# Performance work log

Measured on AMD Instinct MI355X. Metric: run time of the kernel, lower is better.

## Reference

```python
import jax, jax.numpy as jnp
import numpy as np

B, NV, CIN, C = 1, 40000, 128, 64
D, H, W = 19, 200, 176  # sparse_shape = output_shape[1:4] + [1,0,0]
EPS = 1e-3
DN = ('NCDHW', 'OIDHW', 'NCDHW')


def setup_inputs():
    key = jax.random.key(0)
    ks = jax.random.split(key, 12)
    vf = jax.random.normal(ks[0], (NV, CIN), jnp.float32)
    bi = jnp.zeros((NV, 1), jnp.int32)
    zi = jax.random.randint(ks[1], (NV, 1), 0, D, jnp.int32)
    yi = jax.random.randint(ks[2], (NV, 1), 0, H, jnp.int32)
    xi = jax.random.randint(ks[3], (NV, 1), 0, W, jnp.int32)
    coors = jnp.concatenate([bi, zi, yi, xi], axis=1)  # [batch, z, y, x]
    s = 0.05
    w_sub1 = jax.random.normal(ks[4], (C, CIN, 3, 3, 3), jnp.float32) * s
    w_down1 = jax.random.normal(ks[5], (C, C, 3, 1, 1), jnp.float32) * s
    w_sub2 = jax.random.normal(ks[6], (C, C, 3, 3, 3), jnp.float32) * s
    w_sub3 = jax.random.normal(ks[7], (C, C, 3, 3, 3), jnp.float32) * s
    w_down2 = jax.random.normal(ks[8], (C, C, 3, 1, 1), jnp.float32) * s
    bn_gamma = 1.0 + 0.1 * jax.random.normal(ks[9], (5, C), jnp.float32)
    bn_beta = 0.1 * jax.random.normal(ks[10], (5, C), jnp.float32)
    bn_mean = 0.1 * jax.random.normal(ks[11], (5, C), jnp.float32)
    bn_var = jnp.ones((5, C), jnp.float32)
    return dict(voxel_features=vf, coors=coors, batch_size=1,
                w_sub1=w_sub1, w_down1=w_down1, w_sub2=w_sub2, w_sub3=w_sub3,
                w_down2=w_down2, bn_gamma=bn_gamma, bn_beta=bn_beta,
                bn_mean=bn_mean, bn_var=bn_var)


def _conv(x, w, stride, pad):
    return jax.lax.conv_general_dilated(x, w, stride, pad, dimension_numbers=DN)


def _bnrelu(x, i, mask, g, b, m, v):
    # eval-mode BN on active sites only (inactive sites stay exactly zero -> mask)
    inv = jax.lax.rsqrt(v[i] + EPS)
    y = (x - m[i][None, :, None, None, None]) * (g[i] * inv)[None, :, None, None, None] \
        + b[i][None, :, None, None, None]
    return jnp.maximum(y, 0.0) * mask


def _forward(voxel_features, coors, batch_size, w_sub1, w_down1, w_sub2, w_sub3,
             w_down2, bn_gamma, bn_beta, bn_mean, bn_var):
    bi, zi, yi, xi = coors[:, 0], coors[:, 1], coors[:, 2], coors[:, 3]
    # scn.InputLayer: scatter (sum duplicates) active voxel features into dense grid
    dense = jnp.zeros((batch_size, D, H, W, CIN), voxel_features.dtype)
    dense = dense.at[bi, zi, yi, xi].add(voxel_features)
    x = jnp.transpose(dense, (0, 4, 1, 2, 3))  # NCDHW
    mask = jnp.zeros((batch_size, D, H, W), voxel_features.dtype)
    mask = mask.at[bi, zi, yi, xi].set(1.0)[:, None]  # [B,1,D,H,W] active sites
    ones_k = jnp.ones((1, 1, 3, 1, 1), x.dtype)
    pad1 = ((1, 1), (1, 1), (1, 1))
    bn = (bn_gamma, bn_beta, bn_mean, bn_var)
    # SubmanifoldConvolution(128->64, k3) + BNReLU : output only at active sites
    x = _bnrelu(_conv(x, w_sub1, (1, 1, 1), pad1) * mask, 0, mask, *bn)
    # Convolution 64->64 kernel (3,1,1) stride (2,1,1): new active set = any input in window
    x = _conv(x, w_down1, (2, 1, 1), 'VALID')
    mask = (_conv(mask, ones_k, (2, 1, 1), 'VALID') > 0).astype(x.dtype)
    x = _bnrelu(x, 1, mask, *bn)
    # two more submanifold convs
    x = _bnrelu(_conv(x, w_sub2, (1, 1, 1), pad1) * mask, 2, mask, *bn)
    x = _bnrelu(_conv(x, w_sub3, (1, 1, 1), pad1) * mask, 3, mask, *bn)
    # second strided conv
    x = _conv(x, w_down2, (2, 1, 1), 'VALID')
    mask = (_conv(mask, ones_k, (2, 1, 1), 'VALID') > 0).astype(x.dtype)
    x = _bnrelu(x, 4, mask, *bn)
    # SparseToDense then view(N, C*D, H, W)
    Nb, Cc, Dd, Hh, Ww = x.shape
    return x.reshape(Nb, Cc * Dd, Hh, Ww)


def reference(voxel_features, coors, batch_size, w_sub1, w_down1, w_sub2, w_sub3,
              w_down2, bn_gamma, bn_beta, bn_mean, bn_var):
    return _forward(voxel_features, coors, batch_size, w_sub1, w_down1, w_sub2,
                    w_sub3, w_down2, bn_gamma, bn_beta, bn_mean, bn_var)
```

## Files before the change

kernel.cpp:

```cpp
#include <hip/hip_runtime.h>

typedef float floatx4 __attribute__((ext_vector_type(4)));
typedef _Float16 f16x8 __attribute__((ext_vector_type(8)));

#define D0_ 19
#define H0_ 200
#define W0_ 176
#define HW_ (H0_*W0_)
#define NCELL0 (D0_*HW_)
#define D1_ 9
#define NCELL1 (D1_*HW_)
#define D2_ 4
#define NCELL2 (D2_*HW_)
#define NV_ 40000
#define CAP0 40000
#define CAP1 80000
#define CAP2 140800
#define EPS_ 1e-3f

typedef __attribute__((address_space(1))) const unsigned int* gas_t;
typedef __attribute__((address_space(3))) unsigned int* las_t;

__device__ __forceinline__ short f2h(float f){
    _Float16 h = (_Float16)f;
    short s; __builtin_memcpy(&s, &h, 2); return s;
}

__device__ __forceinline__ void repack_one(const float* w, short* Bout, int i,
                                           int KCsrc, int kshift, int NSP){
    int k = i >> 6, n = i & 63;
    int j = k >> kshift;
    int ci = k & (KCsrc - 1);
    short val = f2h(w[(n * KCsrc + ci) * NSP + j]);
    int chunk = k >> 5, lanehi = (k >> 3) & 3, jj = k & 7;
    int nt = n >> 4, lane = lanehi * 16 + (n & 15);
    Bout[((chunk * 4 + nt) * 64 + lane) * 8 + jj] = val;
}

#define RP1 (3456*64)
#define RP2 (1728*64)
#define RPD (192*64)

__global__ void k_prep(const float* w1, const float* w2, const float* w3,
                       const float* wd1, const float* wd2,
                       short* B1, short* B2, short* B3, short* Bd1, short* Bd2,
                       const float* g, const float* b, const float* m, const float* v,
                       float* scale, float* shift){
    int i = blockIdx.x * 256 + threadIdx.x;
    if (i < RP1){ repack_one(w1, B1, i, 128, 7, 27); return; }
    i -= RP1;
    if (i < RP2){ repack_one(w2, B2, i, 64, 6, 27); return; }
    i -= RP2;
    if (i < RP2){ repack_one(w3, B3, i, 64, 6, 27); return; }
    i -= RP2;
    if (i < RPD){ repack_one(wd1, Bd1, i, 64, 6, 3); return; }
    i -= RPD;
    if (i < RPD){ repack_one(wd2, Bd2, i, 64, 6, 3); return; }
    i -= RPD;
    if (i < 5*64){
        float s = g[i] / sqrtf(v[i] + EPS_);
        scale[i] = s;
        shift[i] = b[i] - m[i] * s;
    }
}
#define PREP_TOT (RP1 + 2*RP2 + 2*RPD + 5*64)

__global__ void k_count(const int* coors, int* cntg){
    int v = blockIdx.x * 256 + threadIdx.x;
    if (v >= NV_) return;
    int z = coors[v*4+1], y = coors[v*4+2], x = coors[v*4+3];
    atomicAdd(&cntg[(z*H0_ + y)*W0_ + x], 1);
}

__device__ __forceinline__ int blk_rank(bool act, int* cnt, int& r_out){
    unsigned long long mask = __ballot(act);
    int lane = threadIdx.x & 63, wid = threadIdx.x >> 6;
    int wrank = __popcll(mask & ((1ull << lane) - 1));
    __shared__ int ws[4];
    __shared__ int blkbase;
    if (lane == 0) ws[wid] = __popcll(mask);
    __syncthreads();
    if (threadIdx.x == 0){
        int t0 = ws[0], t1 = ws[1], t2 = ws[2], t3 = ws[3];
        int tot = t0 + t1 + t2 + t3;
        blkbase = tot ? atomicAdd(cnt, tot) : 0;
        ws[0] = 0; ws[1] = t0; ws[2] = t0 + t1; ws[3] = t0 + t1 + t2;
    }
    __syncthreads();
    r_out = blkbase + ws[wid] + wrank;
    return 0;
}

__global__ void k_compact0(const int* cntg, int* idx0, int* list0, int* cnt0){
    int c = blockIdx.x * 256 + threadIdx.x;
    bool act = (c < NCELL0) && (cntg[c] > 0);
    int r; blk_rank(act, cnt0, r);
    if (c >= NCELL0) return;
    if (act){
        idx0[c] = r;
        int z = c / HW_; int rem = c - z * HW_;
        int y = rem / W0_; int x = rem - y * W0_;
        list0[r] = (z << 16) | (y << 8) | x;
    } else idx0[c] = -1;
}

__global__ void k_compact_dn(const int* idxsrc, int* idxdst, int* listdst, int* cnt,
                             int ncell){
    int c = blockIdx.x * 256 + threadIdx.x;
    bool act = false;
    int d = 0, y = 0, x = 0;
    if (c < ncell){
        d = c / HW_; int rem = c - d * HW_;
        y = rem / W0_; x = rem - y * W0_;
        #pragma unroll
        for (int j = 0; j < 3; ++j)
            act = act || (idxsrc[((2*d + j)*H0_ + y)*W0_ + x] >= 0);
    }
    int r; blk_rank(act, cnt, r);
    if (c >= ncell) return;
    if (act){
        idxdst[c] = r;
        listdst[r] = (d << 16) | (y << 8) | x;
    } else idxdst[c] = -1;
}

__global__ void k_scatter(const float* vf, const int* coors, const int* cntg,
                          const int* idx0, float* feat0f){
    int u = blockIdx.x * 256 + threadIdx.x;
    if (u >= NV_ * 32) return;
    int v = u >> 5, c4 = u & 31;
    int z = coors[v*4+1], y = coors[v*4+2], x = coors[v*4+3];
    int cell = (z*H0_ + y)*W0_ + x;
    int row = idx0[cell];
    float4 s = ((const float4*)(vf + (long)v * 128))[c4];
    float* dst = feat0f + (long)row * 128 + c4 * 4;
    if (cntg[cell] == 1){
        *(float4*)dst = s;
    } else {
        atomicAdd(dst+0, s.x); atomicAdd(dst+1, s.y);
        atomicAdd(dst+2, s.z); atomicAdd(dst+3, s.w);
    }
}

__global__ void k_convert(const float* f, short* b, const int* cntp){
    int n8 = cntp[0] * 16;
    int i = blockIdx.x * 256 + threadIdx.x;
    if (i >= n8) return;
    float4 a = ((const float4*)f)[i*2], c = ((const float4*)f)[i*2+1];
    short o[8] = { f2h(a.x), f2h(a.y), f2h(a.z), f2h(a.w),
                   f2h(c.x), f2h(c.y), f2h(c.z), f2h(c.w) };
    ((int4*)b)[i] = *(int4*)o;
}

__global__ void k_nbrs(const int* list0, const int* list1, const int* list2,
                       const int* idx0, const int* idx1,
                       int* nbr0T, int* nbr1T, int* dnb1T, int* dnb2T,
                       const int* counters){
    int job = blockIdx.z;
    int j = blockIdx.y;
    int site = blockIdx.x * 256 + threadIdx.x;
    if (job < 2){
        int M = counters[job];
        if (site >= M) return;
        const int* list = job ? list1 : list0;
        const int* idxg = job ? idx1 : idx0;
        int Dd = job ? D1_ : D0_;
        int cap = job ? CAP1 : CAP0;
        int cell = list[site];
        int z = cell >> 16, y = (cell >> 8) & 255, x = cell & 255;
        int nz = z + j/9 - 1, ny = y + (j/3)%3 - 1, nx = x + j%3 - 1;
        int r = -1;
        if ((unsigned)nz < (unsigned)Dd && (unsigned)ny < H0_ && (unsigned)nx < W0_)
            r = idxg[(nz*H0_ + ny)*W0_ + nx];
        (job ? nbr1T : nbr0T)[j * cap + site] = r;
    } else {
        if (j >= 3) return;
        int lvl = job - 2;
        int M = counters[lvl + 1];
        if (site >= M) return;
        const int* list = lvl ? list2 : list1;
        const int* idxg = lvl ? idx1 : idx0;
        int cap = lvl ? CAP2 : CAP1;
        int cell = list[site];
        int d = cell >> 16, y = (cell >> 8) & 255, x = cell & 255;
        (lvl ? dnb2T : dnb1T)[j * cap + site] = idxg[((2*d + j)*H0_ + y)*W0_ + x];
    }
}

template<int NNBR, int NCH, bool FINAL>
__global__ __launch_bounds__(256) void k_gemm(
    const short* __restrict__ featA, const int* __restrict__ nbrT, int nstride,
    const short* __restrict__ Bs, short* __restrict__ out,
    const int* __restrict__ cntp,
    const float* __restrict__ scale, const float* __restrict__ shift,
    const int* __restrict__ list, float* __restrict__ dout)
{
    __shared__ short Blds[2][NCH*4*512];
    int M = *cntp;
    int m0 = blockIdx.x * 64;
    if (m0 >= M) return;
    int tid = threadIdx.x;
    int wave = tid >> 6, lane = tid & 63;
    int m16 = lane & 15;
    int koff = (lane >> 4) * 8;
    const int ROWS = NCH * 32;
    const int FPW = NCH;

    int row = m0 + wave * 16 + m16;
    bool ok = row < M;

    floatx4 acc[4] = {};
    f16x8 A[2][NCH];
    const f16x8 z8 = {0,0,0,0,0,0,0,0};

    auto stageB = [&](int j, int b){
        #pragma unroll
        for (int f = 0; f < FPW; ++f){
            int frag = wave * FPW + f;
            const short* g = Bs + (((long)j * NCH * 4 + frag) * 64 + lane) * 8;
            __builtin_amdgcn_global_load_lds((gas_t)g, (las_t)&Blds[b][frag * 512],
                                             16, 0, 0);
        }
    };
    auto loadA1 = [&](f16x8* dst, int r, int kc){
        dst[kc] = (r >= 0) ? *(const f16x8*)(featA + (long)r*ROWS + koff + kc*32) : z8;
    };

    int rc = ok ? nbrT[row] : -1;
    stageB(0, 0);
    #pragma unroll
    for (int kc = 0; kc < NCH; ++kc) loadA1(A[0], rc, kc);
    int rb = (NNBR > 1 && ok) ? nbrT[nstride + row] : -1;
    int ra = -1;
    __syncthreads();

    #pragma unroll
    for (int t = 0; t < NNBR; ++t){
        if (t + 1 < NNBR){
            stageB(t + 1, (t + 1) & 1);
            #pragma unroll
            for (int kc = 0; kc < NCH; ++kc) loadA1(A[(t+1)&1], rb, kc);
        }
        if (t + 2 < NNBR)
            ra = ok ? nbrT[(t+2)*nstride + row] : -1;
        if (__ballot(rc >= 0) != 0){
            const short* Bb = Blds[t & 1];
            #pragma unroll
            for (int kc = 0; kc < NCH; ++kc){
                f16x8 b[4];
                #pragma unroll
                for (int nt = 0; nt < 4; ++nt)
                    b[nt] = *(const f16x8*)&Bb[((kc*4 + nt) * 64 + lane) * 8];
                f16x8 a = A[t&1][kc];
                #pragma unroll
                for (int nt = 0; nt < 4; ++nt)
                    acc[nt] = __builtin_amdgcn_mfma_f32_16x16x32_f16(a, b[nt], acc[nt], 0, 0, 0);
            }
        }
        rc = rb; rb = ra;
        __syncthreads();
    }

    int n16 = lane & 15;
    int mb = m0 + wave * 16 + (lane >> 4) * 4;
    #pragma unroll
    for (int nt = 0; nt < 4; ++nt){
        int n = nt * 16 + n16;
        float sc = scale[n], sh = shift[n];
        #pragma unroll
        for (int r = 0; r < 4; ++r){
            int site = mb + r;
            if (site < M){
                float y = fmaxf(acc[nt][r] * sc + sh, 0.f);
                if (FINAL){
                    int cell = list[site];
                    int d = cell >> 16, yy = (cell >> 8) & 255, xx = cell & 255;
                    dout[((n*4 + d)*H0_ + yy)*W0_ + xx] = y;
                } else {
                    out[(long)site*64 + n] = f2h(y);
                }
            }
        }
    }
}

extern "C" void kernel_launch(void* const* d_in, const int* in_sizes, int n_in,
                              void* d_out, int out_size, void* d_ws, size_t ws_size,
                              hipStream_t stream){
    const float* vf   = (const float*)d_in[0];
    const int*   coors= (const int*)  d_in[1];
    const float* w1   = (const float*)d_in[3];
    const float* wd1  = (const float*)d_in[4];
    const float* w2   = (const float*)d_in[5];
    const float* w3   = (const float*)d_in[6];
    const float* wd2  = (const float*)d_in[7];
    const float* bng  = (const float*)d_in[8];
    const float* bnb  = (const float*)d_in[9];
    const float* bnm  = (const float*)d_in[10];
    const float* bnv  = (const float*)d_in[11];
    float* dout = (float*)d_out;

    char* ws = (char*)d_ws;
    size_t off = 0;
    auto alloc = [&](size_t bytes)->char* {
        char* p = ws + off;
        off += (bytes + 255) & ~(size_t)255;
        return p;
    };

    int*   counters = (int*)  alloc(256);
    int*   cntg     = (int*)  alloc((size_t)NCELL0 * 4);
    int*   idx0     = (int*)  alloc((size_t)NCELL0 * 4);
    int*   idx1     = (int*)  alloc((size_t)NCELL1 * 4);
    int*   idx2     = (int*)  alloc((size_t)NCELL2 * 4);
    int*   list0    = (int*)  alloc((size_t)CAP0 * 4);
    int*   list1    = (int*)  alloc((size_t)CAP1 * 4);
    int*   list2    = (int*)  alloc((size_t)CAP2 * 4);
    float* feat0f   = (float*)alloc((size_t)CAP0 * 128 * 4);
    short* feat0h   = (short*)alloc((size_t)CAP0 * 128 * 2);
    short* feat1    = (short*)alloc((size_t)CAP0 * 64 * 2);
    short* featd1   = (short*)alloc((size_t)CAP1 * 64 * 2);
    short* feat2    = (short*)alloc((size_t)CAP1 * 64 * 2);
    short* feat3    = (short*)alloc((size_t)CAP1 * 64 * 2);
    int*   nbr0T    = (int*)  alloc((size_t)CAP0 * 27 * 4);
    int*   nbr1T    = (int*)  alloc((size_t)CAP1 * 27 * 4);
    int*   dnb1T    = (int*)  alloc((size_t)CAP1 * 3 * 4);
    int*   dnb2T    = (int*)  alloc((size_t)CAP2 * 3 * 4);
    short* B1  = (short*)alloc((size_t)3456 * 64 * 2);
    short* B2  = (short*)alloc((size_t)1728 * 64 * 2);
    short* B3  = (short*)alloc((size_t)1728 * 64 * 2);
    short* Bd1 = (short*)alloc((size_t)192 * 64 * 2);
    short* Bd2 = (short*)alloc((size_t)192 * 64 * 2);
    float* bnscale = (float*)alloc(5 * 64 * 4);
    float* bnshift = (float*)alloc(5 * 64 * 4);

    hipMemsetAsync(counters, 0, 256 + (size_t)NCELL0 * 4, stream);
    hipMemsetAsync(feat0f, 0, (size_t)CAP0 * 128 * 4, stream);
    hipMemsetAsync(dout, 0, (size_t)out_size * 4, stream);

    k_prep<<<(PREP_TOT + 255)/256, 256, 0, stream>>>(w1, w2, w3, wd1, wd2,
        B1, B2, B3, Bd1, Bd2, bng, bnb, bnm, bnv, bnscale, bnshift);

    k_count<<<(NV_ + 255)/256, 256, 0, stream>>>(coors, cntg);
    k_compact0<<<(NCELL0 + 255)/256, 256, 0, stream>>>(cntg, idx0, list0, counters + 0);
    k_scatter<<<(NV_*32 + 255)/256, 256, 0, stream>>>(vf, coors, cntg, idx0, feat0f);
    k_convert<<<(CAP0*16 + 255)/256, 256, 0, stream>>>(feat0f, feat0h, counters + 0);
    k_compact_dn<<<(NCELL1 + 255)/256, 256, 0, stream>>>(idx0, idx1, list1, counters + 1, NCELL1);
    k_compact_dn<<<(NCELL2 + 255)/256, 256, 0, stream>>>(idx1, idx2, list2, counters + 2, NCELL2);

    dim3 gn((CAP2 + 255)/256, 27, 4);
    k_nbrs<<<gn, 256, 0, stream>>>(list0, list1, list2, idx0, idx1,
                                   nbr0T, nbr1T, dnb1T, dnb2T, counters);

    k_gemm<27,4,false><<<(CAP0+63)/64, 256, 0, stream>>>(feat0h, nbr0T, CAP0, B1, feat1,
        counters + 0, bnscale + 0,   bnshift + 0,   nullptr, nullptr);
    k_gemm<3,2,false><<<(CAP1+63)/64, 256, 0, stream>>>(feat1, dnb1T, CAP1, Bd1, featd1,
        counters + 1, bnscale + 64,  bnshift + 64,  nullptr, nullptr);
    k_gemm<27,2,false><<<(CAP1+63)/64, 256, 0, stream>>>(featd1, nbr1T, CAP1, B2, feat2,
        counters + 1, bnscale + 128, bnshift + 128, nullptr, nullptr);
    k_gemm<27,2,false><<<(CAP1+63)/64, 256, 0, stream>>>(feat2, nbr1T, CAP1, B3, feat3,
        counters + 1, bnscale + 192, bnshift + 192, nullptr, nullptr);
    k_gemm<3,2,true><<<(CAP2+63)/64, 256, 0, stream>>>(feat3, dnb2T, CAP2, Bd2, nullptr,
        counters + 2, bnscale + 256, bnshift + 256, list2, dout);
}
```

Measured before the change: 318.0 us.

## Compute neighbor indices inline in GEMM kernels and fold voxel counting into prep

Removes the separate neighbor-table kernel and its index tables. Each GEMM now computes neighbor indices on the fly from the site's coordinates and the dense index grid, using a 3-deep A-register pipeline so the index lookup runs ahead of the feature load. The voxel-count atomics are merged into the weight-repack prep kernel, saving one launch. In exchange, the 27-tap index lookups are recomputed in each of the three submanifold GEMMs (the two level-1 convs share the same neighbors), and the lookup latency now sits inside the GEMM loop. More A registers are also live per thread.

```diff
diff --git a/kernel.cpp b/kernel.cpp
--- a/kernel.cpp
+++ b/kernel.cpp
@@ -45,7 +45,8 @@
                        const float* wd1, const float* wd2,
                        short* B1, short* B2, short* B3, short* Bd1, short* Bd2,
                        const float* g, const float* b, const float* m, const float* v,
-                       float* scale, float* shift){
+                       float* scale, float* shift,
+                       const int* coors, int* cntg){
     int i = blockIdx.x * 256 + threadIdx.x;
     if (i < RP1){ repack_one(w1, B1, i, 128, 7, 27); return; }
     i -= RP1;
@@ -61,16 +62,15 @@
         float s = g[i] / sqrtf(v[i] + EPS_);
         scale[i] = s;
         shift[i] = b[i] - m[i] * s;
-    }
-}
-#define PREP_TOT (RP1 + 2*RP2 + 2*RPD + 5*64)
-
-__global__ void k_count(const int* coors, int* cntg){
-    int v = blockIdx.x * 256 + threadIdx.x;
-    if (v >= NV_) return;
-    int z = coors[v*4+1], y = coors[v*4+2], x = coors[v*4+3];
-    atomicAdd(&cntg[(z*H0_ + y)*W0_ + x], 1);
-}
+        return;
+    }
+    i -= 5*64;
+    if (i < NV_){
+        int z = coors[i*4+1], y = coors[i*4+2], x = coors[i*4+3];
+        atomicAdd(&cntg[(z*H0_ + y)*W0_ + x], 1);
+    }
+}
+#define PREP_TOT (RP1 + 2*RP2 + 2*RPD + 5*64 + NV_)
 
 __device__ __forceinline__ int blk_rank(bool act, int* cnt, int& r_out){
     unsigned long long mask = __ballot(act);
@@ -152,50 +152,17 @@
     ((int4*)b)[i] = *(int4*)o;
 }
 
-__global__ void k_nbrs(const int* list0, const int* list1, const int* list2,
-                       const int* idx0, const int* idx1,
-                       int* nbr0T, int* nbr1T, int* dnb1T, int* dnb2T,
-                       const int* counters){
-    int job = blockIdx.z;
-    int j = blockIdx.y;
-    int site = blockIdx.x * 256 + threadIdx.x;
-    if (job < 2){
-        int M = counters[job];
-        if (site >= M) return;
-        const int* list = job ? list1 : list0;
-        const int* idxg = job ? idx1 : idx0;
-        int Dd = job ? D1_ : D0_;
-        int cap = job ? CAP1 : CAP0;
-        int cell = list[site];
-        int z = cell >> 16, y = (cell >> 8) & 255, x = cell & 255;
-        int nz = z + j/9 - 1, ny = y + (j/3)%3 - 1, nx = x + j%3 - 1;
-        int r = -1;
-        if ((unsigned)nz < (unsigned)Dd && (unsigned)ny < H0_ && (unsigned)nx < W0_)
-            r = idxg[(nz*H0_ + ny)*W0_ + nx];
-        (job ? nbr1T : nbr0T)[j * cap + site] = r;
-    } else {
-        if (j >= 3) return;
-        int lvl = job - 2;
-        int M = counters[lvl + 1];
-        if (site >= M) return;
-        const int* list = lvl ? list2 : list1;
-        const int* idxg = lvl ? idx1 : idx0;
-        int cap = lvl ? CAP2 : CAP1;
-        int cell = list[site];
-        int d = cell >> 16, y = (cell >> 8) & 255, x = cell & 255;
-        (lvl ? dnb2T : dnb1T)[j * cap + site] = idxg[((2*d + j)*H0_ + y)*W0_ + x];
-    }
-}
-
-template<int NNBR, int NCH, bool FINAL>
-__global__ __launch_bounds__(256) void k_gemm(
-    const short* __restrict__ featA, const int* __restrict__ nbrT, int nstride,
+template<int NCH>
+__global__ __launch_bounds__(256) void k_gemm27(
+    const short* __restrict__ featA, const int* __restrict__ list,
+    const int* __restrict__ idxg, int Dd,
     const short* __restrict__ Bs, short* __restrict__ out,
     const int* __restrict__ cntp,
-    const float* __restrict__ scale, const float* __restrict__ shift,
-    const int* __restrict__ list, float* __restrict__ dout)
+    const float* __restrict__ scale, const float* __restrict__ shift)
 {
     __shared__ short Blds[2][NCH*4*512];
+    constexpr int NT = 27;
+    const int ROWS = NCH * 32;
     int M = *cntp;
     int m0 = blockIdx.x * 64;
     if (m0 >= M) return;
@@ -203,47 +170,50 @@
     int wave = tid >> 6, lane = tid & 63;
     int m16 = lane & 15;
     int koff = (lane >> 4) * 8;
-    const int ROWS = NCH * 32;
-    const int FPW = NCH;
 
     int row = m0 + wave * 16 + m16;
     bool ok = row < M;
+    int cell = ok ? list[row] : 0xFF0000;
+    int z = cell >> 16, y = (cell >> 8) & 255, x = cell & 255;
 
     floatx4 acc[4] = {};
-    f16x8 A[2][NCH];
+    f16x8 A[3][NCH];
     const f16x8 z8 = {0,0,0,0,0,0,0,0};
 
     auto stageB = [&](int j, int b){
         #pragma unroll
-        for (int f = 0; f < FPW; ++f){
-            int frag = wave * FPW + f;
+        for (int f = 0; f < NCH; ++f){
+            int frag = wave * NCH + f;
             const short* g = Bs + (((long)j * NCH * 4 + frag) * 64 + lane) * 8;
             __builtin_amdgcn_global_load_lds((gas_t)g, (las_t)&Blds[b][frag * 512],
                                              16, 0, 0);
         }
     };
-    auto loadA1 = [&](f16x8* dst, int r, int kc){
-        dst[kc] = (r >= 0) ? *(const f16x8*)(featA + (long)r*ROWS + koff + kc*32) : z8;
-    };
-
-    int rc = ok ? nbrT[row] : -1;
+    auto getR = [&](int t)->int{
+        int nz = z + t/9 - 1, ny = y + (t/3)%3 - 1, nx = x + t%3 - 1;
+        int r = -1;
+        if ((unsigned)nz < (unsigned)Dd && (unsigned)ny < H0_ && (unsigned)nx < W0_)
+            r = idxg[(nz*H0_ + ny)*W0_ + nx];
+        return r;
+    };
+    auto loadA = [&](f16x8* dst, int r){
+        #pragma unroll
+        for (int kc = 0; kc < NCH; ++kc)
+            dst[kc] = (r >= 0) ? *(const f16x8*)(featA + (long)r*ROWS + koff + kc*32) : z8;
+    };
+
+    int r0 = getR(0), r1 = getR(1), r2 = getR(2);
     stageB(0, 0);
+    loadA(A[0], r0);
+    loadA(A[1], r1);
+    __syncthreads();
+
     #pragma unroll
-    for (int kc = 0; kc < NCH; ++kc) loadA1(A[0], rc, kc);
-    int rb = (NNBR > 1 && ok) ? nbrT[nstride + row] : -1;
-    int ra = -1;
-    __syncthreads();
-
-    #pragma unroll
-    for (int t = 0; t < NNBR; ++t){
-        if (t + 1 < NNBR){
-            stageB(t + 1, (t + 1) & 1);
-            #pragma unroll
-            for (int kc = 0; kc < NCH; ++kc) loadA1(A[(t+1)&1], rb, kc);
-        }
-        if (t + 2 < NNBR)
-            ra = ok ? nbrT[(t+2)*nstride + row] : -1;
-        if (__ballot(rc >= 0) != 0){
+    for (int t = 0; t < NT; ++t){
+        if (t + 1 < NT) stageB(t + 1, (t + 1) & 1);
+        if (t + 2 < NT) loadA(A[(t + 2) % 3], r2);
+        int rn = (t + 3 < NT) ? getR(t + 3) : -1;
+        if (__ballot(r0 >= 0) != 0){
             const short* Bb = Blds[t & 1];
             #pragma unroll
             for (int kc = 0; kc < NCH; ++kc){
@@ -251,13 +221,13 @@
                 #pragma unroll
                 for (int nt = 0; nt < 4; ++nt)
                     b[nt] = *(const f16x8*)&Bb[((kc*4 + nt) * 64 + lane) * 8];
-                f16x8 a = A[t&1][kc];
+                f16x8 a = A[t % 3][kc];
                 #pragma unroll
                 for (int nt = 0; nt < 4; ++nt)
                     acc[nt] = __builtin_amdgcn_mfma_f32_16x16x32_f16(a, b[nt], acc[nt], 0, 0, 0);
             }
         }
-        rc = rb; rb = ra;
+        r0 = r1; r1 = r2; r2 = rn;
         __syncthreads();
     }
 
@@ -270,14 +240,109 @@
         #pragma unroll
         for (int r = 0; r < 4; ++r){
             int site = mb + r;
+            if (site < M)
+                out[(long)site*64 + n] = f2h(fmaxf(acc[nt][r] * sc + sh, 0.f));
+        }
+    }
+}
+
+template<bool FINAL>
+__global__ __launch_bounds__(256) void k_gemmdn(
+    const short* __restrict__ featA, const int* __restrict__ list,
+    const int* __restrict__ idxg, int parentD,
+    const short* __restrict__ Bs, short* __restrict__ out,
+    const int* __restrict__ cntp,
+    const float* __restrict__ scale, const float* __restrict__ shift,
+    float* __restrict__ dout)
+{
+    __shared__ short Blds[2][2*4*512];
+    constexpr int NT = 3;
+    const int ROWS = 64;
+    int M = *cntp;
+    int m0 = blockIdx.x * 64;
+    if (m0 >= M) return;
+    int tid = threadIdx.x;
+    int wave = tid >> 6, lane = tid & 63;
+    int m16 = lane & 15;
+    int koff = (lane >> 4) * 8;
+
+    int row = m0 + wave * 16 + m16;
+    bool ok = row < M;
+    int cell = ok ? list[row] : 0;
+    int d = ok ? (cell >> 16) : 300;
+    int y = (cell >> 8) & 255, x = cell & 255;
+
+    floatx4 acc[4] = {};
+    f16x8 A[3][2];
+    const f16x8 z8 = {0,0,0,0,0,0,0,0};
+
+    auto stageB = [&](int j, int b){
+        #pragma unroll
+        for (int f = 0; f < 2; ++f){
+            int frag = wave * 2 + f;
+            const short* g = Bs + (((long)j * 8 + frag) * 64 + lane) * 8;
+            __builtin_amdgcn_global_load_lds((gas_t)g, (las_t)&Blds[b][frag * 512],
+                                             16, 0, 0);
+        }
+    };
+    auto getR = [&](int t)->int{
+        int pz = 2*d + t;
+        int r = -1;
+        if ((unsigned)pz < (unsigned)parentD)
+            r = idxg[(pz*H0_ + y)*W0_ + x];
+        return r;
+    };
+    auto loadA = [&](f16x8* dst, int r){
+        #pragma unroll
+        for (int kc = 0; kc < 2; ++kc)
+            dst[kc] = (r >= 0) ? *(const f16x8*)(featA + (long)r*ROWS + koff + kc*32) : z8;
+    };
+
+    int r0 = getR(0), r1 = getR(1), r2 = getR(2);
+    stageB(0, 0);
+    loadA(A[0], r0);
+    loadA(A[1], r1);
+    __syncthreads();
+
+    #pragma unroll
+    for (int t = 0; t < NT; ++t){
+        if (t + 1 < NT) stageB(t + 1, (t + 1) & 1);
+        if (t + 2 < NT) loadA(A[(t + 2) % 3], r2);
+        if (__ballot(r0 >= 0) != 0){
+            const short* Bb = Blds[t & 1];
+            #pragma unroll
+            for (int kc = 0; kc < 2; ++kc){
+                f16x8 b[4];
+                #pragma unroll
+                for (int nt = 0; nt < 4; ++nt)
+                    b[nt] = *(const f16x8*)&Bb[((kc*4 + nt) * 64 + lane) * 8];
+                f16x8 a = A[t % 3][kc];
+                #pragma unroll
+                for (int nt = 0; nt < 4; ++nt)
+                    acc[nt] = __builtin_amdgcn_mfma_f32_16x16x32_f16(a, b[nt], acc[nt], 0, 0, 0);
+            }
+        }
+        r0 = r1; r1 = r2; r2 = -1;
+        __syncthreads();
+    }
+
+    int n16 = lane & 15;
+    int mb = m0 + wave * 16 + (lane >> 4) * 4;
+    #pragma unroll
+    for (int nt = 0; nt < 4; ++nt){
+        int n = nt * 16 + n16;
+        float sc = scale[n], sh = shift[n];
+        #pragma unroll
+        for (int r = 0; r < 4; ++r){
+            int site = mb + r;
             if (site < M){
-                float y = fmaxf(acc[nt][r] * sc + sh, 0.f);
+                float yv = fmaxf(acc[nt][r] * sc + sh, 0.f);
                 if (FINAL){
-                    int cell = list[site];
-                    int d = cell >> 16, yy = (cell >> 8) & 255, xx = cell & 255;
-                    dout[((n*4 + d)*H0_ + yy)*W0_ + xx] = y;
+                    int c2 = list[site];
+                    int dd = c2 >> 16, yy = (c2 >> 8) & 255, xx = c2 & 255;
+                    dout[((n*4 + dd)*H0_ + yy)*W0_ + xx] = yv;
                 } else {
-                    out[(long)site*64 + n] = f2h(y);
+                    out[(long)site*64 + n] = f2h(yv);
                 }
             }
         }
@@ -322,10 +387,6 @@
     short* featd1   = (short*)alloc((size_t)CAP1 * 64 * 2);
     short* feat2    = (short*)alloc((size_t)CAP1 * 64 * 2);
     short* feat3    = (short*)alloc((size_t)CAP1 * 64 * 2);
-    int*   nbr0T    = (int*)  alloc((size_t)CAP0 * 27 * 4);
-    int*   nbr1T    = (int*)  alloc((size_t)CAP1 * 27 * 4);
-    int*   dnb1T    = (int*)  alloc((size_t)CAP1 * 3 * 4);
-    int*   dnb2T    = (int*)  alloc((size_t)CAP2 * 3 * 4);
     short* B1  = (short*)alloc((size_t)3456 * 64 * 2);
     short* B2  = (short*)alloc((size_t)1728 * 64 * 2);
     short* B3  = (short*)alloc((size_t)1728 * 64 * 2);
@@ -339,27 +400,22 @@
     hipMemsetAsync(dout, 0, (size_t)out_size * 4, stream);
 
     k_prep<<<(PREP_TOT + 255)/256, 256, 0, stream>>>(w1, w2, w3, wd1, wd2,
-        B1, B2, B3, Bd1, Bd2, bng, bnb, bnm, bnv, bnscale, bnshift);
-
-    k_count<<<(NV_ + 255)/256, 256, 0, stream>>>(coors, cntg);
+        B1, B2, B3, Bd1, Bd2, bng, bnb, bnm, bnv, bnscale, bnshift, coors, cntg);
+
     k_compact0<<<(NCELL0 + 255)/256, 256, 0, stream>>>(cntg, idx0, list0, counters + 0);
     k_scatter<<<(NV_*32 + 255)/256, 256, 0, stream>>>(vf, coors, cntg, idx0, feat0f);
     k_convert<<<(CAP0*16 + 255)/256, 256, 0, stream>>>(feat0f, feat0h, counters + 0);
     k_compact_dn<<<(NCELL1 + 255)/256, 256, 0, stream>>>(idx0, idx1, list1, counters + 1, NCELL1);
     k_compact_dn<<<(NCELL2 + 255)/256, 256, 0, stream>>>(idx1, idx2, list2, counters + 2, NCELL2);
 
-    dim3 gn((CAP2 + 255)/256, 27, 4);
-    k_nbrs<<<gn, 256, 0, stream>>>(list0, list1, list2, idx0, idx1,
-                                   nbr0T, nbr1T, dnb1T, dnb2T, counters);
-
-    k_gemm<27,4,false><<<(CAP0+63)/64, 256, 0, stream>>>(feat0h, nbr0T, CAP0, B1, feat1,
-        counters + 0, bnscale + 0,   bnshift + 0,   nullptr, nullptr);
-    k_gemm<3,2,false><<<(CAP1+63)/64, 256, 0, stream>>>(feat1, dnb1T, CAP1, Bd1, featd1,
-        counters + 1, bnscale + 64,  bnshift + 64,  nullptr, nullptr);
-    k_gemm<27,2,false><<<(CAP1+63)/64, 256, 0, stream>>>(featd1, nbr1T, CAP1, B2, feat2,
-        counters + 1, bnscale + 128, bnshift + 128, nullptr, nullptr);
-    k_gemm<27,2,false><<<(CAP1+63)/64, 256, 0, stream>>>(feat2, nbr1T, CAP1, B3, feat3,
-        counters + 1, bnscale + 192, bnshift + 192, nullptr, nullptr);
-    k_gemm<3,2,true><<<(CAP2+63)/64, 256, 0, stream>>>(feat3, dnb2T, CAP2, Bd2, nullptr,
-        counters + 2, bnscale + 256, bnshift + 256, list2, dout);
-}
+    k_gemm27<4><<<(CAP0+63)/64, 256, 0, stream>>>(feat0h, list0, idx0, D0_, B1, feat1,
+        counters + 0, bnscale + 0,   bnshift + 0);
+    k_gemmdn<false><<<(CAP1+63)/64, 256, 0, stream>>>(feat1, list1, idx0, D0_, Bd1, featd1,
+        counters + 1, bnscale + 64,  bnshift + 64,  nullptr);
+    k_gemm27<2><<<(CAP1+63)/64, 256, 0, stream>>>(featd1, list1, idx1, D1_, B2, feat2,
+        counters + 1, bnscale + 128, bnshift + 128);
+    k_gemm27<2><<<(CAP1+63)/64, 256, 0, stream>>>(feat2, list1, idx1, D1_, B3, feat3,
+        counters + 1, bnscale + 192, bnshift + 192);
+    k_gemmdn<true><<<(CAP2+63)/64, 256, 0, stream>>>(feat3, list2, idx1, D1_, Bd2, nullptr,
+        counters + 2, bnscale + 256, bnshift + 256, dout);
+}
```

New measurement: 288.9 us. -9.1%, faster.
